# Optimization experiments

Hardware: AMD Instinct MI355X
Metric: run time of the kernel (lower is better)

The kernel has to match this reference:

```python
import jax, jax.numpy as jnp
import numpy as np

BS, NUM_PATCH, N_VARS, PATCH_LEN, D_MODEL = 32, 64, 321, 12, 128
TIME_RATIO, FREQ_RATIO = 0.5, 0.4


def setup_inputs() -> dict:
    key = jax.random.key(0)
    ks = jax.random.split(key, 7)
    x = jax.random.normal(ks[0], (BS, NUM_PATCH, N_VARS, PATCH_LEN), jnp.float32)
    W_in = jax.random.normal(ks[1], (PATCH_LEN, D_MODEL), jnp.float32) / np.sqrt(PATCH_LEN)
    b_in = jnp.zeros((D_MODEL,), jnp.float32)
    W_out = jax.random.normal(ks[2], (D_MODEL, PATCH_LEN), jnp.float32) / np.sqrt(D_MODEL)
    b_out = jnp.zeros((PATCH_LEN,), jnp.float32)
    # nn.Parameter(torch.zeros(1,1,1)) in the original; use small random scalars so grads are non-trivial
    time_mask_token = jax.random.normal(ks[3], (), jnp.float32) * 0.02
    freq_mask_token = jax.random.normal(ks[4], (), jnp.float32) * 0.02
    return {"x": x, "W_in": W_in, "b_in": b_in, "W_out": W_out, "b_out": b_out,
            "time_mask_token": time_mask_token, "freq_mask_token": freq_mask_token}


def _scatter_mask(idx, num_patch):
    # idx: [bs, n_vars, k] patch indices to mask (set False). Returns bool [bs, num_patch, n_vars].
    bs, nv, k = idx.shape
    m = jnp.ones((bs, num_patch, nv), dtype=bool)
    b = jnp.arange(bs)[:, None, None]
    v = jnp.arange(nv)[None, :, None]
    return m.at[b, idx, v].set(False)


def reference(x, W_in, b_in, W_out, b_out, time_mask_token, freq_mask_token):
    bs, num_patch, n_vars, patch_len = x.shape

    # patch2emb applied per token (equivalent to the gather-encode path since the
    # projection is pointwise per patch): [bs, np, nv, d_model]
    emb = jnp.einsum('bpvl,ld->bpvd', x, W_in) + b_in

    # ---- time masking: mask patches with highest coefficient of variation ----
    cv = jnp.std(x, axis=-1, ddof=1) / (jnp.mean(x, axis=-1) + 1e-6)  # [bs, np, nv]
    k_t = int(num_patch * TIME_RATIO)
    _, idx_t = jax.lax.top_k(jnp.transpose(cv, (0, 2, 1)), k_t)       # [bs, nv, k_t]
    mask_t = _scatter_mask(idx_t, num_patch)                           # True = keep
    tokens_t = jnp.where(mask_t[..., None], emb, time_mask_token)
    out_t = jnp.einsum('bpvd,dl->bpvl', tokens_t, W_out) + b_out

    # ---- freq masking: mask patches with lowest mean FFT magnitude ----
    mag = jnp.abs(jnp.fft.rfft(x, axis=-1))                            # [bs, np, nv, pl//2+1]
    score = mag.mean(axis=-1)                                          # [bs, np, nv]
    k_f = int(num_patch * FREQ_RATIO)
    _, idx_f = jax.lax.top_k(-jnp.transpose(score, (0, 2, 1)), k_f)    # smallest scores
    mask_f = _scatter_mask(idx_f, num_patch)
    tokens_f = jnp.where(mask_f[..., None], emb, freq_mask_token)
    out_f = jnp.einsum('bpvd,dl->bpvl', tokens_f, W_out) + b_out

    return out_t * 0.5 + out_f * 0.5
```

## Files before the change

kernel.cpp:

```cpp
#include <hip/hip_runtime.h>
#include <math.h>

constexpr int BS = 32, NV = 321, PL = 12, DM = 128;
constexpr int KT = 32;
constexpr int KF = 25;
constexpr int VB = 4;
constexpr int NCHUNK = 81;
constexpr int SST = 72;

__device__ __forceinline__ unsigned ord(float f) {
  unsigned u = __float_as_uint(f);
  return ((int)u < 0) ? ~u : (u | 0x80000000u);
}

__global__ __launch_bounds__(256) void fused_kernel(
    const float* __restrict__ x, const float* __restrict__ W_in,
    const float* __restrict__ b_in, const float* __restrict__ W_out,
    const float* __restrict__ b_out, const float* __restrict__ tt,
    const float* __restrict__ ft, float* __restrict__ out) {
  __shared__ float scv[VB * SST];
  __shared__ float sfs[VB * SST];
  __shared__ __align__(16) float spp[192];
  __shared__ unsigned long long smT[VB], smF[VB];

  const int t = threadIdx.x;
  const int chunk = blockIdx.x;
  const int b = blockIdx.y;
  const int v0 = chunk * VB;
  const bool full = (chunk < 80);
  const int p = t >> 2;
  const int vv = t & 3;
  const bool valid = full || (vv == 0);

  float xr[12];
  if (valid) {
    const float4* src =
        (const float4*)(x + (((size_t)(b * 64 + p) * NV) + v0 + vv) * PL);
    float4 a = src[0], bb = src[1], c = src[2];
    xr[0] = a.x;  xr[1] = a.y;  xr[2] = a.z;  xr[3] = a.w;
    xr[4] = bb.x; xr[5] = bb.y; xr[6] = bb.z; xr[7] = bb.w;
    xr[8] = c.x;  xr[9] = c.y;  xr[10] = c.z; xr[11] = c.w;
  }

  if (t < 144) {
    const int i = t / 12, l = t - (t / 12) * 12;
    const float4* Wi = (const float4*)(W_in + i * DM);
    float s = 0.f;
#pragma unroll 8
    for (int d4 = 0; d4 < 32; ++d4) {
      float4 a = Wi[d4];
      const float* wo = W_out + d4 * 48 + l;
      s += a.x * wo[0] + a.y * wo[12] + a.z * wo[24] + a.w * wo[36];
    }
    spp[t] = s;
  } else if (t < 168) {
    const int l = (t - 144) % 12;
    float cs = 0.f, cb = 0.f;
#pragma unroll 8
    for (int d = 0; d < DM; ++d) {
      float w = W_out[d * 12 + l];
      cs += w;
      cb += b_in[d] * w;
    }
    if (t < 156) {
      spp[144 + l] = cb;
      spp[156 + l] = tt[0] * cs;
    } else {
      spp[168 + l] = ft[0] * cs;
    }
  } else if (t < 180) {
    spp[180 + (t - 168)] = b_out[t - 168];
  }

  const float H = 0.86602540378443864676f;
  if (valid) {
    const float* xv = xr;
    float s = 0.f;
#pragma unroll
    for (int i = 0; i < 12; ++i) s += xv[i];
    const float m = s * (1.0f / 12.0f);
    float ss = 0.f;
#pragma unroll
    for (int i = 0; i < 12; ++i) {
      float d = xv[i] - m;
      ss += d * d;
    }
    const float cv = sqrtf(ss * (1.0f / 11.0f)) / (m + 1e-6f);

    const float e1 = xv[1] + xv[11], e2 = xv[2] + xv[10], e3 = xv[3] + xv[9],
                e4 = xv[4] + xv[8], e5 = xv[5] + xv[7];
    const float o1 = xv[1] - xv[11], o2 = xv[2] - xv[10], o3 = xv[3] - xv[9],
                o4 = xv[4] - xv[8], o5 = xv[5] - xv[7];
    float mag = fabsf(xv[0] + xv[6] + e1 + e2 + e3 + e4 + e5);
    float re = xv[0] - xv[6] + H * (e1 - e5) + 0.5f * (e2 - e4);
    float im = 0.5f * (o1 + o5) + H * (o2 + o4) + o3;
    mag += sqrtf(re * re + im * im);
    re = xv[0] + xv[6] + 0.5f * (e1 + e5) - 0.5f * (e2 + e4) - e3;
    im = H * (o1 + o2 - o4 - o5);
    mag += sqrtf(re * re + im * im);
    re = xv[0] - xv[6] - e2 + e4;
    im = o1 - o3 + o5;
    mag += sqrtf(re * re + im * im);
    re = xv[0] + xv[6] - 0.5f * (e1 + e2 + e4 + e5) + e3;
    im = H * (o1 - o2 + o4 - o5);
    mag += sqrtf(re * re + im * im);
    re = xv[0] - xv[6] + H * (e5 - e1) + 0.5f * (e2 - e4);
    im = 0.5f * (o1 + o5) - H * (o2 + o4) + o3;
    mag += sqrtf(re * re + im * im);
    re = xv[0] + xv[6] - e1 + e2 - e3 + e4 - e5;
    mag += fabsf(re);
    const float fs = mag * (1.0f / 7.0f);

    scv[vv * SST + p] = cv;
    sfs[vv * SST + p] = fs;
  }
  __syncthreads();

  const int wv = t >> 6, lane = t & 63;
  if (full || wv == 0) {
    const unsigned ut = ord(scv[wv * SST + lane]);
    const unsigned uf = ~ord(sfs[wv * SST + lane]);
    unsigned tht = 0, thf = 0;
#pragma unroll
    for (int bit = 31; bit >= 0; --bit) {
      const unsigned ct = tht | (1u << bit);
      const unsigned cf = thf | (1u << bit);
      const unsigned long long bt = __ballot(ut >= ct);
      const unsigned long long bf = __ballot(uf >= cf);
      if (__popcll(bt) >= KT) tht = ct;
      if (__popcll(bf) >= KF) thf = cf;
    }
    const unsigned long long pre = (1ull << lane) - 1ull;
    const int gt_t = __popcll(__ballot(ut > tht));
    const int rt = __popcll(__ballot(ut == tht) & pre);
    const bool masked_t = (ut > tht) || ((ut == tht) && (rt < KT - gt_t));
    const int gt_f = __popcll(__ballot(uf > thf));
    const int rf = __popcll(__ballot(uf == thf) & pre);
    const bool masked_f = (uf > thf) || ((uf == thf) && (rf < KF - gt_f));
    const unsigned long long bkt = __ballot(!masked_t);
    const unsigned long long bkf = __ballot(!masked_f);
    if (lane == 0) {
      smT[wv] = bkt;
      smF[wv] = bkf;
    }
  }
  __syncthreads();

  const bool kt = (smT[vv] >> p) & 1ull;
  const bool kf = (smF[vv] >> p) & 1ull;
  float E[12];
#pragma unroll
  for (int l = 0; l < 12; ++l) E[l] = spp[144 + l];
  const float4* M4 = (const float4*)spp;
#pragma unroll
  for (int i = 0; i < 12; ++i) {
    const float4 m0 = M4[i * 3], m1 = M4[i * 3 + 1], m2 = M4[i * 3 + 2];
    const float a = xr[i];
    E[0] += a * m0.x;  E[1] += a * m0.y;  E[2] += a * m0.z;  E[3] += a * m0.w;
    E[4] += a * m1.x;  E[5] += a * m1.y;  E[6] += a * m1.z;  E[7] += a * m1.w;
    E[8] += a * m2.x;  E[9] += a * m2.y;  E[10] += a * m2.z; E[11] += a * m2.w;
  }
  if (valid) {
    float o[12];
#pragma unroll
    for (int l = 0; l < 12; ++l) {
      const float at = kt ? E[l] : spp[156 + l];
      const float af = kf ? E[l] : spp[168 + l];
      o[l] = 0.5f * (at + af) + spp[180 + l];
    }
    float* op = out + (((size_t)(b * 64 + p) * NV) + v0 + vv) * PL;
    ((float4*)op)[0] = make_float4(o[0], o[1], o[2], o[3]);
    ((float4*)op)[1] = make_float4(o[4], o[5], o[6], o[7]);
    ((float4*)op)[2] = make_float4(o[8], o[9], o[10], o[11]);
  }
}

extern "C" void kernel_launch(void* const* d_in, const int* in_sizes, int n_in,
                              void* d_out, int out_size, void* d_ws,
                              size_t ws_size, hipStream_t stream) {
  const float* x = (const float*)d_in[0];
  const float* W_in = (const float*)d_in[1];
  const float* b_in = (const float*)d_in[2];
  const float* W_out = (const float*)d_in[3];
  const float* b_out = (const float*)d_in[4];
  const float* tt = (const float*)d_in[5];
  const float* ft = (const float*)d_in[6];
  float* out = (float*)d_out;

  hipLaunchKernelGGL(fused_kernel, dim3(NCHUNK, BS), dim3(256), 0, stream, x,
                     W_in, b_in, W_out, b_out, tt, ft, out);
}
```

Baseline: 122.6 us.

## Hoist weight folding into a separate prep kernel and read folded matrix from global

The folded W_in·W_out matrix and bias/mask constants were computed redundantly by every block. They are now computed once by a single-block prep kernel into workspace, and the main kernel reads them directly from global memory (cached, uniform addresses). The embedding projection is also moved before the final barrier so it overlaps with the top-k ballot work, and launch bounds request higher occupancy. It adds a second kernel launch and relies on cache-served uniform global loads instead of LDS.

After: 137.1 us. +11.9%, slower.

```diff
diff --git a/kernel.cpp b/kernel.cpp
--- a/kernel.cpp
+++ b/kernel.cpp
@@ -13,14 +13,50 @@
   return ((int)u < 0) ? ~u : (u | 0x80000000u);
 }
 
-__global__ __launch_bounds__(256) void fused_kernel(
-    const float* __restrict__ x, const float* __restrict__ W_in,
-    const float* __restrict__ b_in, const float* __restrict__ W_out,
-    const float* __restrict__ b_out, const float* __restrict__ tt,
-    const float* __restrict__ ft, float* __restrict__ out) {
+__global__ void prep_kernel(const float* __restrict__ W_in,
+                            const float* __restrict__ b_in,
+                            const float* __restrict__ W_out,
+                            const float* __restrict__ b_out,
+                            const float* __restrict__ tt,
+                            const float* __restrict__ ft,
+                            float* __restrict__ prep) {
+  int t = threadIdx.x;
+  if (t < 144) {
+    int i = t / 12, l = t % 12;
+    const float4* Wi = (const float4*)(W_in + i * DM);
+    float s = 0.f;
+#pragma unroll 8
+    for (int d4 = 0; d4 < 32; ++d4) {
+      float4 a = Wi[d4];
+      const float* wo = W_out + d4 * 48 + l;
+      s += a.x * wo[0] + a.y * wo[12] + a.z * wo[24] + a.w * wo[36];
+    }
+    prep[t] = s;
+  } else if (t < 168) {
+    int l = (t - 144) % 12;
+    float cs = 0.f, cb = 0.f;
+#pragma unroll 8
+    for (int d = 0; d < DM; ++d) {
+      float w = W_out[d * 12 + l];
+      cs += w;
+      cb += b_in[d] * w;
+    }
+    if (t < 156) {
+      prep[144 + l] = cb;
+      prep[156 + l] = tt[0] * cs;
+    } else {
+      prep[168 + l] = ft[0] * cs;
+    }
+  } else if (t < 180) {
+    prep[180 + (t - 168)] = b_out[t - 168];
+  }
+}
+
+__global__ __launch_bounds__(256, 8) void fused_kernel(
+    const float* __restrict__ x, const float* __restrict__ prep,
+    float* __restrict__ out) {
   __shared__ float scv[VB * SST];
   __shared__ float sfs[VB * SST];
-  __shared__ __align__(16) float spp[192];
   __shared__ unsigned long long smT[VB], smF[VB];
 
   const int t = threadIdx.x;
@@ -40,36 +76,6 @@
     xr[0] = a.x;  xr[1] = a.y;  xr[2] = a.z;  xr[3] = a.w;
     xr[4] = bb.x; xr[5] = bb.y; xr[6] = bb.z; xr[7] = bb.w;
     xr[8] = c.x;  xr[9] = c.y;  xr[10] = c.z; xr[11] = c.w;
-  }
-
-  if (t < 144) {
-    const int i = t / 12, l = t - (t / 12) * 12;
-    const float4* Wi = (const float4*)(W_in + i * DM);
-    float s = 0.f;
-#pragma unroll 8
-    for (int d4 = 0; d4 < 32; ++d4) {
-      float4 a = Wi[d4];
-      const float* wo = W_out + d4 * 48 + l;
-      s += a.x * wo[0] + a.y * wo[12] + a.z * wo[24] + a.w * wo[36];
-    }
-    spp[t] = s;
-  } else if (t < 168) {
-    const int l = (t - 144) % 12;
-    float cs = 0.f, cb = 0.f;
-#pragma unroll 8
-    for (int d = 0; d < DM; ++d) {
-      float w = W_out[d * 12 + l];
-      cs += w;
-      cb += b_in[d] * w;
-    }
-    if (t < 156) {
-      spp[144 + l] = cb;
-      spp[156 + l] = tt[0] * cs;
-    } else {
-      spp[168 + l] = ft[0] * cs;
-    }
-  } else if (t < 180) {
-    spp[180 + (t - 168)] = b_out[t - 168];
   }
 
   const float H = 0.86602540378443864676f;
@@ -144,29 +150,27 @@
       smF[wv] = bkf;
     }
   }
+
+  float E[12];
+#pragma unroll
+  for (int l = 0; l < 12; ++l) E[l] = prep[144 + l];
+#pragma unroll
+  for (int i = 0; i < 12; ++i) {
+    const float a = xr[i];
+#pragma unroll
+    for (int l = 0; l < 12; ++l) E[l] += a * prep[i * 12 + l];
+  }
   __syncthreads();
 
-  const bool kt = (smT[vv] >> p) & 1ull;
-  const bool kf = (smF[vv] >> p) & 1ull;
-  float E[12];
-#pragma unroll
-  for (int l = 0; l < 12; ++l) E[l] = spp[144 + l];
-  const float4* M4 = (const float4*)spp;
-#pragma unroll
-  for (int i = 0; i < 12; ++i) {
-    const float4 m0 = M4[i * 3], m1 = M4[i * 3 + 1], m2 = M4[i * 3 + 2];
-    const float a = xr[i];
-    E[0] += a * m0.x;  E[1] += a * m0.y;  E[2] += a * m0.z;  E[3] += a * m0.w;
-    E[4] += a * m1.x;  E[5] += a * m1.y;  E[6] += a * m1.z;  E[7] += a * m1.w;
-    E[8] += a * m2.x;  E[9] += a * m2.y;  E[10] += a * m2.z; E[11] += a * m2.w;
-  }
   if (valid) {
+    const bool kt = (smT[vv] >> p) & 1ull;
+    const bool kf = (smF[vv] >> p) & 1ull;
     float o[12];
 #pragma unroll
     for (int l = 0; l < 12; ++l) {
-      const float at = kt ? E[l] : spp[156 + l];
-      const float af = kf ? E[l] : spp[168 + l];
-      o[l] = 0.5f * (at + af) + spp[180 + l];
+      const float at = kt ? E[l] : prep[156 + l];
+      const float af = kf ? E[l] : prep[168 + l];
+      o[l] = 0.5f * (at + af) + prep[180 + l];
     }
     float* op = out + (((size_t)(b * 64 + p) * NV) + v0 + vv) * PL;
     ((float4*)op)[0] = make_float4(o[0], o[1], o[2], o[3]);
@@ -186,7 +190,10 @@
   const float* tt = (const float*)d_in[5];
   const float* ft = (const float*)d_in[6];
   float* out = (float*)d_out;
+  float* prep = (float*)d_ws;
 
+  hipLaunchKernelGGL(prep_kernel, dim3(1), dim3(192), 0, stream, W_in, b_in,
+                     W_out, b_out, tt, ft, prep);
   hipLaunchKernelGGL(fused_kernel, dim3(NCHUNK, BS), dim3(256), 0, stream, x,
-                     W_in, b_in, W_out, b_out, tt, ft, out);
+                     prep, out);
 }
```

## Split fused kernel into score, rank, and decode kernels with coalesced row access

Applied to the files above, without the earlier changes.

Replaces the single fused kernel with three launches. The first computes per-token CV and FFT scores with coalesced row-wise reads and also precomputes the folded weights once. The second ranks the scores per (batch, variable) with wave ballots and writes keep bitmasks. The third re-reads x and writes the output coalesced. The goal is to avoid the strided 4-variable access pattern and the redundant per-block weight precompute, at the cost of reading x twice, round-tripping scores through global memory, and two extra launches.

Result: faster. 118.9 us (-3.0%).

```diff
diff --git a/kernel.cpp b/kernel.cpp
--- a/kernel.cpp
+++ b/kernel.cpp
@@ -1,153 +1,164 @@
 #include <hip/hip_runtime.h>
 #include <math.h>
 
-constexpr int BS = 32, NV = 321, PL = 12, DM = 128;
+constexpr int BS = 32, NP = 64, NV = 321, PL = 12, DM = 128;
 constexpr int KT = 32;
 constexpr int KF = 25;
-constexpr int VB = 4;
-constexpr int NCHUNK = 81;
-constexpr int SST = 72;
+constexpr int ROWF = NV * PL;
+
+constexpr size_t SCORES_OFF = 0;
+constexpr size_t MASKS_OFF = (size_t)BS * NP * NV * 8;
+constexpr size_t PREP_OFF = MASKS_OFF + (size_t)BS * NV * 16;
 
 __device__ __forceinline__ unsigned ord(float f) {
   unsigned u = __float_as_uint(f);
   return ((int)u < 0) ? ~u : (u | 0x80000000u);
 }
 
-__global__ __launch_bounds__(256) void fused_kernel(
+__device__ __forceinline__ void compute_scores(const float* xv, float& cv,
+                                               float& fs) {
+  const float H = 0.86602540378443864676f;
+  float s = 0.f;
+#pragma unroll
+  for (int i = 0; i < 12; ++i) s += xv[i];
+  const float m = s * (1.0f / 12.0f);
+  float ss = 0.f;
+#pragma unroll
+  for (int i = 0; i < 12; ++i) {
+    float d = xv[i] - m;
+    ss += d * d;
+  }
+  cv = sqrtf(ss * (1.0f / 11.0f)) / (m + 1e-6f);
+  const float e1 = xv[1] + xv[11], e2 = xv[2] + xv[10], e3 = xv[3] + xv[9],
+              e4 = xv[4] + xv[8], e5 = xv[5] + xv[7];
+  const float o1 = xv[1] - xv[11], o2 = xv[2] - xv[10], o3 = xv[3] - xv[9],
+              o4 = xv[4] - xv[8], o5 = xv[5] - xv[7];
+  float mag = fabsf(xv[0] + xv[6] + e1 + e2 + e3 + e4 + e5);
+  float re = xv[0] - xv[6] + H * (e1 - e5) + 0.5f * (e2 - e4);
+  float im = 0.5f * (o1 + o5) + H * (o2 + o4) + o3;
+  mag += sqrtf(re * re + im * im);
+  re = xv[0] + xv[6] + 0.5f * (e1 + e5) - 0.5f * (e2 + e4) - e3;
+  im = H * (o1 + o2 - o4 - o5);
+  mag += sqrtf(re * re + im * im);
+  re = xv[0] - xv[6] - e2 + e4;
+  im = o1 - o3 + o5;
+  mag += sqrtf(re * re + im * im);
+  re = xv[0] + xv[6] - 0.5f * (e1 + e2 + e4 + e5) + e3;
+  im = H * (o1 - o2 + o4 - o5);
+  mag += sqrtf(re * re + im * im);
+  re = xv[0] - xv[6] + H * (e5 - e1) + 0.5f * (e2 - e4);
+  im = 0.5f * (o1 + o5) - H * (o2 + o4) + o3;
+  mag += sqrtf(re * re + im * im);
+  re = xv[0] + xv[6] - e1 + e2 - e3 + e4 - e5;
+  mag += fabsf(re);
+  fs = mag * (1.0f / 7.0f);
+}
+
+__global__ __launch_bounds__(384) void score_prep_kernel(
     const float* __restrict__ x, const float* __restrict__ W_in,
     const float* __restrict__ b_in, const float* __restrict__ W_out,
     const float* __restrict__ b_out, const float* __restrict__ tt,
-    const float* __restrict__ ft, float* __restrict__ out) {
-  __shared__ float scv[VB * SST];
-  __shared__ float sfs[VB * SST];
-  __shared__ __align__(16) float spp[192];
-  __shared__ unsigned long long smT[VB], smF[VB];
-
+    const float* __restrict__ ft, float2* __restrict__ scores,
+    float* __restrict__ prep) {
   const int t = threadIdx.x;
+  if (blockIdx.x == BS * NP) {
+    if (t < 144) {
+      const int i = t / 12, l = t - (t / 12) * 12;
+      const float4* Wi = (const float4*)(W_in + i * DM);
+      float s = 0.f;
+#pragma unroll 8
+      for (int d4 = 0; d4 < 32; ++d4) {
+        float4 a = Wi[d4];
+        const float* wo = W_out + d4 * 48 + l;
+        s += a.x * wo[0] + a.y * wo[12] + a.z * wo[24] + a.w * wo[36];
+      }
+      prep[t] = s;
+    } else if (t < 168) {
+      const int l = (t - 144) % 12;
+      float cs = 0.f, cb = 0.f;
+#pragma unroll 8
+      for (int d = 0; d < DM; ++d) {
+        float w = W_out[d * 12 + l];
+        cs += w;
+        cb += b_in[d] * w;
+      }
+      if (t < 156) {
+        prep[144 + l] = cb;
+        prep[156 + l] = tt[0] * cs;
+      } else {
+        prep[168 + l] = ft[0] * cs;
+      }
+    } else if (t < 180) {
+      prep[180 + (t - 168)] = b_out[t - 168];
+    }
+    return;
+  }
+  if (t >= NV) return;
+  const int bp = blockIdx.x;
+  const float4* src = (const float4*)(x + (size_t)bp * ROWF + t * PL);
+  const float4 a = src[0], b4 = src[1], c4 = src[2];
+  const float xv[12] = {a.x,  a.y,  a.z,  a.w,  b4.x, b4.y,
+                        b4.z, b4.w, c4.x, c4.y, c4.z, c4.w};
+  float cv, fs;
+  compute_scores(xv, cv, fs);
+  scores[(size_t)bp * NV + t] = make_float2(cv, fs);
+}
+
+__global__ __launch_bounds__(256) void rank_kernel(
+    const float2* __restrict__ scores, ulonglong2* __restrict__ masks) {
   const int chunk = blockIdx.x;
   const int b = blockIdx.y;
-  const int v0 = chunk * VB;
-  const bool full = (chunk < 80);
-  const int p = t >> 2;
-  const int vv = t & 3;
-  const bool valid = full || (vv == 0);
-
-  float xr[12];
-  if (valid) {
-    const float4* src =
-        (const float4*)(x + (((size_t)(b * 64 + p) * NV) + v0 + vv) * PL);
-    float4 a = src[0], bb = src[1], c = src[2];
-    xr[0] = a.x;  xr[1] = a.y;  xr[2] = a.z;  xr[3] = a.w;
-    xr[4] = bb.x; xr[5] = bb.y; xr[6] = bb.z; xr[7] = bb.w;
-    xr[8] = c.x;  xr[9] = c.y;  xr[10] = c.z; xr[11] = c.w;
-  }
-
-  if (t < 144) {
-    const int i = t / 12, l = t - (t / 12) * 12;
-    const float4* Wi = (const float4*)(W_in + i * DM);
-    float s = 0.f;
-#pragma unroll 8
-    for (int d4 = 0; d4 < 32; ++d4) {
-      float4 a = Wi[d4];
-      const float* wo = W_out + d4 * 48 + l;
-      s += a.x * wo[0] + a.y * wo[12] + a.z * wo[24] + a.w * wo[36];
+  const int wv = threadIdx.x >> 6, lane = threadIdx.x & 63;
+#pragma unroll
+  for (int h = 0; h < 2; ++h) {
+    const int v = chunk * 8 + wv * 2 + h;
+    if (v < NV) {
+      const float2 s2 = scores[(size_t)(b * 64 + lane) * NV + v];
+      const unsigned ut = ord(s2.x);
+      const unsigned uf = ~ord(s2.y);
+      unsigned tht = 0, thf = 0;
+#pragma unroll
+      for (int bit = 31; bit >= 0; --bit) {
+        const unsigned ct = tht | (1u << bit);
+        const unsigned cf = thf | (1u << bit);
+        const unsigned long long bt = __ballot(ut >= ct);
+        const unsigned long long bf = __ballot(uf >= cf);
+        if (__popcll(bt) >= KT) tht = ct;
+        if (__popcll(bf) >= KF) thf = cf;
+      }
+      const unsigned long long pre = (1ull << lane) - 1ull;
+      const int gt_t = __popcll(__ballot(ut > tht));
+      const int rt = __popcll(__ballot(ut == tht) & pre);
+      const bool masked_t = (ut > tht) || ((ut == tht) && (rt < KT - gt_t));
+      const int gt_f = __popcll(__ballot(uf > thf));
+      const int rf = __popcll(__ballot(uf == thf) & pre);
+      const bool masked_f = (uf > thf) || ((uf == thf) && (rf < KF - gt_f));
+      const unsigned long long bkt = __ballot(!masked_t);
+      const unsigned long long bkf = __ballot(!masked_f);
+      if (lane == 0) masks[b * NV + v] = make_ulonglong2(bkt, bkf);
     }
-    spp[t] = s;
-  } else if (t < 168) {
-    const int l = (t - 144) % 12;
-    float cs = 0.f, cb = 0.f;
-#pragma unroll 8
-    for (int d = 0; d < DM; ++d) {
-      float w = W_out[d * 12 + l];
-      cs += w;
-      cb += b_in[d] * w;
-    }
-    if (t < 156) {
-      spp[144 + l] = cb;
-      spp[156 + l] = tt[0] * cs;
-    } else {
-      spp[168 + l] = ft[0] * cs;
-    }
-  } else if (t < 180) {
-    spp[180 + (t - 168)] = b_out[t - 168];
-  }
-
-  const float H = 0.86602540378443864676f;
-  if (valid) {
-    const float* xv = xr;
-    float s = 0.f;
-#pragma unroll
-    for (int i = 0; i < 12; ++i) s += xv[i];
-    const float m = s * (1.0f / 12.0f);
-    float ss = 0.f;
-#pragma unroll
-    for (int i = 0; i < 12; ++i) {
-      float d = xv[i] - m;
-      ss += d * d;
-    }
-    const float cv = sqrtf(ss * (1.0f / 11.0f)) / (m + 1e-6f);
-
-    const float e1 = xv[1] + xv[11], e2 = xv[2] + xv[10], e3 = xv[3] + xv[9],
-                e4 = xv[4] + xv[8], e5 = xv[5] + xv[7];
-    const float o1 = xv[1] - xv[11], o2 = xv[2] - xv[10], o3 = xv[3] - xv[9],
-                o4 = xv[4] - xv[8], o5 = xv[5] - xv[7];
-    float mag = fabsf(xv[0] + xv[6] + e1 + e2 + e3 + e4 + e5);
-    float re = xv[0] - xv[6] + H * (e1 - e5) + 0.5f * (e2 - e4);
-    float im = 0.5f * (o1 + o5) + H * (o2 + o4) + o3;
-    mag += sqrtf(re * re + im * im);
-    re = xv[0] + xv[6] + 0.5f * (e1 + e5) - 0.5f * (e2 + e4) - e3;
-    im = H * (o1 + o2 - o4 - o5);
-    mag += sqrtf(re * re + im * im);
-    re = xv[0] - xv[6] - e2 + e4;
-    im = o1 - o3 + o5;
-    mag += sqrtf(re * re + im * im);
-    re = xv[0] + xv[6] - 0.5f * (e1 + e2 + e4 + e5) + e3;
-    im = H * (o1 - o2 + o4 - o5);
-    mag += sqrtf(re * re + im * im);
-    re = xv[0] - xv[6] + H * (e5 - e1) + 0.5f * (e2 - e4);
-    im = 0.5f * (o1 + o5) - H * (o2 + o4) + o3;
-    mag += sqrtf(re * re + im * im);
-    re = xv[0] + xv[6] - e1 + e2 - e3 + e4 - e5;
-    mag += fabsf(re);
-    const float fs = mag * (1.0f / 7.0f);
-
-    scv[vv * SST + p] = cv;
-    sfs[vv * SST + p] = fs;
-  }
+  }
+}
+
+__global__ __launch_bounds__(384) void decode_kernel(
+    const float* __restrict__ x, const ulonglong2* __restrict__ masks,
+    const float* __restrict__ prep, float* __restrict__ out) {
+  __shared__ __align__(16) float spp[192];
+  const int t = threadIdx.x;
+  if (t < 192) spp[t] = prep[t];
   __syncthreads();
-
-  const int wv = t >> 6, lane = t & 63;
-  if (full || wv == 0) {
-    const unsigned ut = ord(scv[wv * SST + lane]);
-    const unsigned uf = ~ord(sfs[wv * SST + lane]);
-    unsigned tht = 0, thf = 0;
-#pragma unroll
-    for (int bit = 31; bit >= 0; --bit) {
-      const unsigned ct = tht | (1u << bit);
-      const unsigned cf = thf | (1u << bit);
-      const unsigned long long bt = __ballot(ut >= ct);
-      const unsigned long long bf = __ballot(uf >= cf);
-      if (__popcll(bt) >= KT) tht = ct;
-      if (__popcll(bf) >= KF) thf = cf;
-    }
-    const unsigned long long pre = (1ull << lane) - 1ull;
-    const int gt_t = __popcll(__ballot(ut > tht));
-    const int rt = __popcll(__ballot(ut == tht) & pre);
-    const bool masked_t = (ut > tht) || ((ut == tht) && (rt < KT - gt_t));
-    const int gt_f = __popcll(__ballot(uf > thf));
-    const int rf = __popcll(__ballot(uf == thf) & pre);
-    const bool masked_f = (uf > thf) || ((uf == thf) && (rf < KF - gt_f));
-    const unsigned long long bkt = __ballot(!masked_t);
-    const unsigned long long bkf = __ballot(!masked_f);
-    if (lane == 0) {
-      smT[wv] = bkt;
-      smF[wv] = bkf;
-    }
-  }
-  __syncthreads();
-
-  const bool kt = (smT[vv] >> p) & 1ull;
-  const bool kf = (smF[vv] >> p) & 1ull;
+  if (t >= NV) return;
+  const int bp = blockIdx.x;
+  const int b = bp >> 6, p = bp & 63;
+
+  const float4* src = (const float4*)(x + (size_t)bp * ROWF + t * PL);
+  const float4 a = src[0], b4 = src[1], c4 = src[2];
+  const float xv[12] = {a.x,  a.y,  a.z,  a.w,  b4.x, b4.y,
+                        b4.z, b4.w, c4.x, c4.y, c4.z, c4.w};
+  const ulonglong2 mk = masks[b * NV + t];
+  const bool kt = (mk.x >> p) & 1ull;
+  const bool kf = (mk.y >> p) & 1ull;
+
   float E[12];
 #pragma unroll
   for (int l = 0; l < 12; ++l) E[l] = spp[144 + l];
@@ -155,24 +166,22 @@
 #pragma unroll
   for (int i = 0; i < 12; ++i) {
     const float4 m0 = M4[i * 3], m1 = M4[i * 3 + 1], m2 = M4[i * 3 + 2];
-    const float a = xr[i];
-    E[0] += a * m0.x;  E[1] += a * m0.y;  E[2] += a * m0.z;  E[3] += a * m0.w;
-    E[4] += a * m1.x;  E[5] += a * m1.y;  E[6] += a * m1.z;  E[7] += a * m1.w;
-    E[8] += a * m2.x;  E[9] += a * m2.y;  E[10] += a * m2.z; E[11] += a * m2.w;
-  }
-  if (valid) {
-    float o[12];
-#pragma unroll
-    for (int l = 0; l < 12; ++l) {
-      const float at = kt ? E[l] : spp[156 + l];
-      const float af = kf ? E[l] : spp[168 + l];
-      o[l] = 0.5f * (at + af) + spp[180 + l];
-    }
-    float* op = out + (((size_t)(b * 64 + p) * NV) + v0 + vv) * PL;
-    ((float4*)op)[0] = make_float4(o[0], o[1], o[2], o[3]);
-    ((float4*)op)[1] = make_float4(o[4], o[5], o[6], o[7]);
-    ((float4*)op)[2] = make_float4(o[8], o[9], o[10], o[11]);
-  }
+    const float av = xv[i];
+    E[0] += av * m0.x;  E[1] += av * m0.y;  E[2] += av * m0.z;  E[3] += av * m0.w;
+    E[4] += av * m1.x;  E[5] += av * m1.y;  E[6] += av * m1.z;  E[7] += av * m1.w;
+    E[8] += av * m2.x;  E[9] += av * m2.y;  E[10] += av * m2.z; E[11] += av * m2.w;
+  }
+  float o[12];
+#pragma unroll
+  for (int l = 0; l < 12; ++l) {
+    const float at = kt ? E[l] : spp[156 + l];
+    const float af = kf ? E[l] : spp[168 + l];
+    o[l] = 0.5f * (at + af) + spp[180 + l];
+  }
+  float4* dst = (float4*)(out + (size_t)bp * ROWF + t * PL);
+  dst[0] = make_float4(o[0], o[1], o[2], o[3]);
+  dst[1] = make_float4(o[4], o[5], o[6], o[7]);
+  dst[2] = make_float4(o[8], o[9], o[10], o[11]);
 }
 
 extern "C" void kernel_launch(void* const* d_in, const int* in_sizes, int n_in,
@@ -187,6 +196,14 @@
   const float* ft = (const float*)d_in[6];
   float* out = (float*)d_out;
 
-  hipLaunchKernelGGL(fused_kernel, dim3(NCHUNK, BS), dim3(256), 0, stream, x,
-                     W_in, b_in, W_out, b_out, tt, ft, out);
-}
+  float2* scores = (float2*)((char*)d_ws + SCORES_OFF);
+  ulonglong2* masks = (ulonglong2*)((char*)d_ws + MASKS_OFF);
+  float* prep = (float*)((char*)d_ws + PREP_OFF);
+
+  hipLaunchKernelGGL(score_prep_kernel, dim3(BS * NP + 1), dim3(384), 0,
+                     stream, x, W_in, b_in, W_out, b_out, tt, ft, scores, prep);
+  hipLaunchKernelGGL(rank_kernel, dim3(41, BS), dim3(256), 0, stream, scores,
+                     masks);
+  hipLaunchKernelGGL(decode_kernel, dim3(BS * NP), dim3(384), 0, stream, x,
+                     masks, prep, out);
+}
```
